# Optimization experiments

Measured on AMD Instinct MI355X. Metric: run time of the kernel, lower is better.

## Reference

```python
import jax, jax.numpy as jnp
import numpy as np
import math

B, S, H, DK = 16, 4096, 16, 64
DM = H * DK          # 1024, d_model
QD = 1024            # q_d_model
KVD = 1024           # kv_d_model
MASK_P = 0.85        # randbool probability


def setup_inputs() -> dict:
    key = jax.random.key(0)
    ks = jax.random.split(key, 12)
    s = 0.02
    return {
        "q": jax.random.normal(ks[0], (B, 1, QD), jnp.float32),
        "k": jax.random.normal(ks[1], (B, S, KVD), jnp.float32),
        "v": jax.random.normal(ks[2], (B, S, KVD), jnp.float32),
        "Wq": jax.random.normal(ks[3], (QD, DM), jnp.float32) * s,
        "bq": jnp.zeros((DM,), jnp.float32),
        "Wk": jax.random.normal(ks[4], (KVD, DM), jnp.float32) * s,
        "bk": jnp.zeros((DM,), jnp.float32),
        "Wv": jax.random.normal(ks[5], (KVD, DM), jnp.float32) * s,
        "bv": jnp.zeros((DM,), jnp.float32),
        "Wo": jax.random.normal(ks[6], (DM, QD), jnp.float32) * s,
        "bo": jnp.zeros((QD,), jnp.float32),
        # randbool(shape, p=0.85): True where rand < p -> score zeroed
        "maskfill": jax.random.uniform(ks[7], (B, H, 1, S)) < MASK_P,
    }


def reference(q, k, v, Wq, bq, Wk, bk, Wv, bv, Wo, bo, maskfill):
    bs = q.shape[0]
    # projections -> [B, L, H, DK] -> [B, H, L, DK]
    qh = (q @ Wq + bq).reshape(bs, -1, H, DK).transpose(0, 2, 1, 3)  # [B,H,1,DK]
    kh = (k @ Wk + bk).reshape(bs, -1, H, DK).transpose(0, 2, 1, 3)  # [B,H,S,DK]
    vh = (v @ Wv + bv).reshape(bs, -1, H, DK).transpose(0, 2, 1, 3)  # [B,H,S,DK]

    scores1 = jnp.einsum("bhqd,bhkd->bhqk", qh, kh) / math.sqrt(DK)  # [B,H,1,S]

    # plain path (dropout = identity in eval)
    attn = jax.nn.softmax(scores1, axis=-1)
    out_h = jnp.einsum("bhqk,bhkd->bhqd", attn, vh)                  # [B,H,1,DK]

    # masked path: zero-fill (not -inf) masked raw scores, then softmax
    masked_scores = jnp.where(maskfill, 0.0, scores1)
    mattn = jax.nn.softmax(masked_scores, axis=-1)
    mout_h = jnp.einsum("bhqk,bhkd->bhqd", mattn, vh)

    concat = out_h.transpose(0, 2, 1, 3).reshape(bs, DM)
    mconcat = mout_h.transpose(0, 2, 1, 3).reshape(bs, DM)
    output = concat @ Wo + bo
    masked_output = mconcat @ Wo + bo
    return (output, masked_output)
```

## Files before the change

kernel.cpp:

```cpp
#include <hip/hip_runtime.h>
#include <stdint.h>

#define NB 16
#define NS 4096
#define NH 16
#define NC 1024

#define OFF_QHP   0u
#define OFF_QK    262144u
#define OFF_QB    524288u
#define OFF_SP    524608u
#define OFF_CTXP  532800u
#define OFF_CON   8921408u

__global__ __launch_bounds__(128) void k_qh(
    const float* __restrict__ q, const float* __restrict__ Wq, float* __restrict__ qhp)
{
    __shared__ float qs[64*16];
    int dz = blockIdx.x, cs = blockIdx.y;
    int tid = threadIdx.x;
    int d = dz*128 + tid;
#pragma unroll
    for (int j = 0; j < 2; ++j) {
        int idx = j*128 + tid;
        int b = idx >> 4, c4 = (idx & 15) << 2;
        float4 t = *(const float4*)(q + (size_t)b*NC + cs*64 + c4);
        qs[(c4+0)*16 + b] = t.x; qs[(c4+1)*16 + b] = t.y;
        qs[(c4+2)*16 + b] = t.z; qs[(c4+3)*16 + b] = t.w;
    }
    __syncthreads();
    float acc[16];
#pragma unroll
    for (int b = 0; b < 16; ++b) acc[b] = 0.f;
#pragma unroll 4
    for (int c = 0; c < 64; ++c) {
        float w = Wq[(size_t)(cs*64 + c)*NC + d];
        const float4* qr = (const float4*)(qs + c*16);
        float4 q0 = qr[0], q1 = qr[1], q2 = qr[2], q3 = qr[3];
        acc[0]  = fmaf(w, q0.x, acc[0]);  acc[1]  = fmaf(w, q0.y, acc[1]);
        acc[2]  = fmaf(w, q0.z, acc[2]);  acc[3]  = fmaf(w, q0.w, acc[3]);
        acc[4]  = fmaf(w, q1.x, acc[4]);  acc[5]  = fmaf(w, q1.y, acc[5]);
        acc[6]  = fmaf(w, q1.z, acc[6]);  acc[7]  = fmaf(w, q1.w, acc[7]);
        acc[8]  = fmaf(w, q2.x, acc[8]);  acc[9]  = fmaf(w, q2.y, acc[9]);
        acc[10] = fmaf(w, q2.z, acc[10]); acc[11] = fmaf(w, q2.w, acc[11]);
        acc[12] = fmaf(w, q3.x, acc[12]); acc[13] = fmaf(w, q3.y, acc[13]);
        acc[14] = fmaf(w, q3.z, acc[14]); acc[15] = fmaf(w, q3.w, acc[15]);
    }
#pragma unroll
    for (int b = 0; b < 16; ++b) qhp[((size_t)cs*16 + b)*NC + d] = acc[b];
}

__global__ __launch_bounds__(128) void k_qk(
    const float* __restrict__ qhp, const float* __restrict__ bq,
    const float* __restrict__ Wk, const float* __restrict__ bk,
    float* __restrict__ qko, float* __restrict__ qbv)
{
    int h = blockIdx.x;
    int c = blockIdx.y*128 + threadIdx.x;
    __shared__ float qs[16*64];
    for (int j = 0; j < 8; ++j) {
        int idx = j*128 + threadIdx.x;
        int b = idx >> 6, dd = idx & 63;
        float a = bq[h*64 + dd];
#pragma unroll
        for (int cs = 0; cs < 16; ++cs) a += qhp[((size_t)cs*16 + b)*NC + h*64 + dd];
        qs[idx] = a;
    }
    __syncthreads();
    const float* wr = Wk + (size_t)c*NC + h*64;
    float acc[16];
#pragma unroll
    for (int b = 0; b < 16; ++b) acc[b] = 0.f;
#pragma unroll 4
    for (int d = 0; d < 64; ++d) {
        float w = wr[d];
#pragma unroll
        for (int b = 0; b < 16; ++b) acc[b] = fmaf(qs[b*64 + d], w, acc[b]);
    }
#pragma unroll
    for (int b = 0; b < 16; ++b) qko[((size_t)b*NH + h)*NC + c] = acc[b];
    if (blockIdx.y == 0 && threadIdx.x < 16) {
        int b = threadIdx.x; float a = 0.f;
        for (int d = 0; d < 64; ++d) a = fmaf(qs[b*64 + d], bk[h*64 + d], a);
        qbv[b*NH + h] = a;
    }
}

#define QTS 20
#define SCOMP(BUF, W)                                                          \
    _Pragma("unroll")                                                          \
    for (int j = 0; j < 4; ++j) {                                              \
        const float* qp = qt + ((W)*16 + ph*4 + j)*QTS + hg*4;                 \
        float4 qv = *(const float4*)qp;                                        \
        _Pragma("unroll")                                                      \
        for (int i = 0; i < 8; ++i) {                                          \
            float kc = (j == 0) ? BUF[i].x : (j == 1) ? BUF[i].y               \
                     : (j == 2) ? BUF[i].z : BUF[i].w;                         \
            acc[i][0] = fmaf(kc, qv.x, acc[i][0]);                             \
            acc[i][1] = fmaf(kc, qv.y, acc[i][1]);                             \
            acc[i][2] = fmaf(kc, qv.z, acc[i][2]);                             \
            acc[i][3] = fmaf(kc, qv.w, acc[i][3]);                             \
        }                                                                      \
    }
__global__ __launch_bounds__(512, 2) void k_att(
    const float* __restrict__ kk, const float* __restrict__ vv,
    const float* __restrict__ qkm, const float* __restrict__ qbv,
    const void* __restrict__ mask, float* __restrict__ ctxp, float* __restrict__ Sp)
{
    __shared__ float qt[512*QTS];
    __shared__ float attl[256*32];
    __shared__ float red[8][2][16];
    int sb = blockIdx.x, b = blockIdx.y;
    int tid = threadIdx.x;
    int ph = tid & 3, hg = (tid >> 2) & 3, rg = tid >> 4;
    int srow = sb*256 + rg*8;

    int fl;
    {
        const uint4* mw = (const uint4*)mask;
        unsigned f = 0u, g = 0u;
#pragma unroll
        for (int j = 0; j < 8; ++j) {
            uint4 m4 = mw[j];
            f |= (m4.x == 0x3F800000u) | (m4.y == 0x3F800000u)
               | (m4.z == 0x3F800000u) | (m4.w == 0x3F800000u);
            g |= ((m4.x > 1u) & (m4.x != 0x3F800000u))
               | ((m4.y > 1u) & (m4.y != 0x3F800000u))
               | ((m4.z > 1u) & (m4.z != 0x3F800000u))
               | ((m4.w > 1u) & (m4.w != 0x3F800000u));
        }
        fl = f ? 2 : (g ? 1 : 0);
    }

    const float* kr = kk + ((size_t)b*NS + srow)*NC + ph*4;
    float acc[8][4];
#pragma unroll
    for (int i = 0; i < 8; ++i)
#pragma unroll
        for (int j = 0; j < 4; ++j) acc[i][j] = 0.f;

    for (int cz = 0; cz < 2; ++cz) {
        __syncthreads();
#pragma unroll
        for (int j = 0; j < 16; ++j) {
            int idx = j*512 + tid;
            int h = idx >> 9, c = idx & 511;
            qt[c*QTS + h] = qkm[((size_t)b*NH + h)*NC + cz*512 + c];
        }
        __syncthreads();
        const float* kc0 = kr + cz*512;
        float4 A[8], B[8], T[8];
#pragma unroll
        for (int i = 0; i < 8; ++i) A[i] = *(const float4*)(kc0 + i*NC);
#pragma unroll
        for (int i = 0; i < 8; ++i) B[i] = *(const float4*)(kc0 + i*NC + 16);
        for (int w = 0; w < 32; w += 2) {
            if (w + 2 < 32) {
#pragma unroll
                for (int i = 0; i < 8; ++i)
                    T[i] = *(const float4*)(kc0 + i*NC + (w+2)*16);
            }
            SCOMP(A, w);
            if (w + 3 < 32) {
#pragma unroll
                for (int i = 0; i < 8; ++i)
                    A[i] = *(const float4*)(kc0 + i*NC + (w+3)*16);
            }
            SCOMP(B, (w+1));
#pragma unroll
            for (int i = 0; i < 8; ++i) { B[i] = A[i]; A[i] = T[i]; }
        }
    }
#pragma unroll
    for (int i = 0; i < 8; ++i)
#pragma unroll
        for (int j = 0; j < 4; ++j) {
            acc[i][j] += __shfl_xor(acc[i][j], 1, 64);
            acc[i][j] += __shfl_xor(acc[i][j], 2, 64);
        }
    float d0[4], d1[4];
    if (ph == 0) {
#pragma unroll
        for (int j = 0; j < 4; ++j) { d0[j] = acc[0][j]; d1[j] = acc[1][j]; }
    } else if (ph == 1) {
#pragma unroll
        for (int j = 0; j < 4; ++j) { d0[j] = acc[2][j]; d1[j] = acc[3][j]; }
    } else if (ph == 2) {
#pragma unroll
        for (int j = 0; j < 4; ++j) { d0[j] = acc[4][j]; d1[j] = acc[5][j]; }
    } else {
#pragma unroll
        for (int j = 0; j < 4; ++j) { d0[j] = acc[6][j]; d1[j] = acc[7][j]; }
    }
    int lA = rg*8 + 2*ph, lB = lA + 1;
    int sA = sb*256 + lA, sB = sA + 1;
    unsigned mA = 0, mB = 0;
    if (fl == 1) {
        const uint8_t* mp = (const uint8_t*)mask + (size_t)(b*NH + hg*4)*NS;
#pragma unroll
        for (int j = 0; j < 4; ++j) {
            if (mp[(size_t)j*NS + sA]) mA |= (1u << j);
            if (mp[(size_t)j*NS + sB]) mB |= (1u << j);
        }
    } else if (fl == 2) {
        const float* mp = (const float*)mask + (size_t)(b*NH + hg*4)*NS;
#pragma unroll
        for (int j = 0; j < 4; ++j) {
            if (mp[(size_t)j*NS + sA] != 0.f) mA |= (1u << j);
            if (mp[(size_t)j*NS + sB] != 0.f) mB |= (1u << j);
        }
    } else {
        const int* mp = (const int*)mask + (size_t)(b*NH + hg*4)*NS;
#pragma unroll
        for (int j = 0; j < 4; ++j) {
            if (mp[(size_t)j*NS + sA]) mA |= (1u << j);
            if (mp[(size_t)j*NS + sB]) mB |= (1u << j);
        }
    }
    float p0a[4], p1a[4], p0b[4], p1b[4], r0[4], r1[4];
#pragma unroll
    for (int j = 0; j < 4; ++j) {
        float qb = qbv[b*NH + hg*4 + j];
        float va = (d0[j] + qb) * 0.125f;
        float vb2 = (d1[j] + qb) * 0.125f;
        p0a[j] = __expf(va);  p1a[j] = (mA >> j & 1u) ? 1.0f : p0a[j];
        p0b[j] = __expf(vb2); p1b[j] = (mB >> j & 1u) ? 1.0f : p0b[j];
        r0[j] = p0a[j] + p0b[j];
        r1[j] = p1a[j] + p1b[j];
    }
    {
        int swA = (lA & 7) << 2, swB = (lB & 7) << 2;
        *(float4*)(attl + lA*32 + ((hg*4) ^ swA))        = make_float4(p0a[0], p0a[1], p0a[2], p0a[3]);
        *(float4*)(attl + lA*32 + ((16 + hg*4) ^ swA))   = make_float4(p1a[0], p1a[1], p1a[2], p1a[3]);
        *(float4*)(attl + lB*32 + ((hg*4) ^ swB))        = make_float4(p0b[0], p0b[1], p0b[2], p0b[3]);
        *(float4*)(attl + lB*32 + ((16 + hg*4) ^ swB))   = make_float4(p1b[0], p1b[1], p1b[2], p1b[3]);
    }
#pragma unroll
    for (int j = 0; j < 4; ++j) {
        r0[j] += __shfl_xor(r0[j], 1, 64);  r1[j] += __shfl_xor(r1[j], 1, 64);
        r0[j] += __shfl_xor(r0[j], 2, 64);  r1[j] += __shfl_xor(r1[j], 2, 64);
        r0[j] += __shfl_xor(r0[j], 16, 64); r1[j] += __shfl_xor(r1[j], 16, 64);
        r0[j] += __shfl_xor(r0[j], 32, 64); r1[j] += __shfl_xor(r1[j], 32, 64);
    }
    int wv = tid >> 6;
    if ((tid & 51) == 0) {
#pragma unroll
        for (int j = 0; j < 4; ++j) {
            red[wv][0][hg*4 + j] = r0[j];
            red[wv][1][hg*4 + j] = r1[j];
        }
    }
    __syncthreads();
    if (tid < 32) {
        int pa = tid >> 4, h = tid & 15;
        float a = 0.f;
#pragma unroll
        for (int w8 = 0; w8 < 8; ++w8) a += red[w8][pa][h];
        Sp[((size_t)b*16 + sb)*32 + tid] = a;
    }

    int cq = tid & 255, half = tid >> 8;
    float cacc[16][4];
#pragma unroll
    for (int u = 0; u < 16; ++u)
#pragma unroll
        for (int j = 0; j < 4; ++j) cacc[u][j] = 0.f;
    const float* vb = vv + ((size_t)b*NS + sb*256)*NC + cq*4;
    float4 vr[8], vn[8];
#pragma unroll
    for (int i = 0; i < 8; ++i) vr[i] = *(const float4*)(vb + (size_t)i*NC);
    for (int r0q = 0; r0q < 256; r0q += 8) {
        if (r0q + 8 < 256) {
#pragma unroll
            for (int i = 0; i < 8; ++i)
                vn[i] = *(const float4*)(vb + (size_t)(r0q + 8 + i)*NC);
        }
#pragma unroll
        for (int i = 0; i < 8; ++i) {
            int r = r0q + i;
            const float* ar = attl + r*32;
            int lw = r & 7;
            float4 vcur = vr[i];
#pragma unroll
            for (int g = 0; g < 4; ++g) {
                int G = half*4 + g;
                float4 aw = *(const float4*)(ar + ((G ^ lw) << 2));
                cacc[g*4+0][0] = fmaf(aw.x, vcur.x, cacc[g*4+0][0]);
                cacc[g*4+0][1] = fmaf(aw.x, vcur.y, cacc[g*4+0][1]);
                cacc[g*4+0][2] = fmaf(aw.x, vcur.z, cacc[g*4+0][2]);
                cacc[g*4+0][3] = fmaf(aw.x, vcur.w, cacc[g*4+0][3]);
                cacc[g*4+1][0] = fmaf(aw.y, vcur.x, cacc[g*4+1][0]);
                cacc[g*4+1][1] = fmaf(aw.y, vcur.y, cacc[g*4+1][1]);
                cacc[g*4+1][2] = fmaf(aw.y, vcur.z, cacc[g*4+1][2]);
                cacc[g*4+1][3] = fmaf(aw.y, vcur.w, cacc[g*4+1][3]);
                cacc[g*4+2][0] = fmaf(aw.z, vcur.x, cacc[g*4+2][0]);
                cacc[g*4+2][1] = fmaf(aw.z, vcur.y, cacc[g*4+2][1]);
                cacc[g*4+2][2] = fmaf(aw.z, vcur.z, cacc[g*4+2][2]);
                cacc[g*4+2][3] = fmaf(aw.z, vcur.w, cacc[g*4+2][3]);
                cacc[g*4+3][0] = fmaf(aw.w, vcur.x, cacc[g*4+3][0]);
                cacc[g*4+3][1] = fmaf(aw.w, vcur.y, cacc[g*4+3][1]);
                cacc[g*4+3][2] = fmaf(aw.w, vcur.z, cacc[g*4+3][2]);
                cacc[g*4+3][3] = fmaf(aw.w, vcur.w, cacc[g*4+3][3]);
            }
        }
#pragma unroll
        for (int i = 0; i < 8; ++i) vr[i] = vn[i];
    }
#pragma unroll
    for (int gh = 0; gh < 16; ++gh) {
        *(float4*)(ctxp + ((((size_t)sb*2 + half)*NB + b)*NH + gh)*NC + cq*4)
            = make_float4(cacc[gh][0], cacc[gh][1], cacc[gh][2], cacc[gh][3]);
    }
}

__global__ __launch_bounds__(256) void k_outhN(
    const float* __restrict__ ctxp, const float* __restrict__ Sp,
    const float* __restrict__ Wv, const float* __restrict__ bv,
    float* __restrict__ con)
{
    int b = blockIdx.y, p = blockIdx.z;
    int dx = blockIdx.x;
    int d = dx*256 + threadIdx.x;
    int h0 = dx*4;
    __shared__ float cl[4*NC];
    float Sinv[4];
#pragma unroll
    for (int j = 0; j < 4; ++j) {
        float a = 0.f;
        for (int sb = 0; sb < 16; ++sb)
            a += Sp[((size_t)b*16 + sb)*32 + p*16 + h0 + j];
        Sinv[j] = 1.f / a;
    }
#pragma unroll
    for (int hh = 0; hh < 4; ++hh) {
        for (int cc = threadIdx.x; cc < NC; cc += 256) {
            float a = 0.f;
#pragma unroll
            for (int ss = 0; ss < 16; ++ss)
                a += ctxp[((((size_t)ss*2 + p)*NB + b)*NH + h0 + hh)*NC + cc];
            cl[hh*NC + cc] = a * Sinv[hh];
        }
    }
    __syncthreads();
    const float* c2 = cl + ((threadIdx.x >> 6) << 10);
    float a0=0.f,a1=0.f,a2=0.f,a3=0.f;
    for (int c = 0; c < NC; c += 4) {
        a0 = fmaf(c2[c+0], Wv[(size_t)(c+0)*NC + d], a0);
        a1 = fmaf(c2[c+1], Wv[(size_t)(c+1)*NC + d], a1);
        a2 = fmaf(c2[c+2], Wv[(size_t)(c+2)*NC + d], a2);
        a3 = fmaf(c2[c+3], Wv[(size_t)(c+3)*NC + d], a3);
    }
    con[((size_t)p*NB + b)*NC + d] = (a0+a1)+(a2+a3) + bv[d];
}

__global__ __launch_bounds__(256) void k_out(
    const float* __restrict__ con, const float* __restrict__ Wo,
    const float* __restrict__ bo, float* __restrict__ out)
{
    int b = blockIdx.y, p = blockIdx.z;
    int o = blockIdx.x*256 + threadIdx.x;
    __shared__ float cl[NC];
    for (int i = threadIdx.x; i < NC; i += 256)
        cl[i] = con[((size_t)p*NB + b)*NC + i];
    __syncthreads();
    float a0=0.f,a1=0.f,a2=0.f,a3=0.f;
    for (int m = 0; m < NC; m += 4) {
        a0 = fmaf(cl[m+0], Wo[(size_t)(m+0)*NC + o], a0);
        a1 = fmaf(cl[m+1], Wo[(size_t)(m+1)*NC + o], a1);
        a2 = fmaf(cl[m+2], Wo[(size_t)(m+2)*NC + o], a2);
        a3 = fmaf(cl[m+3], Wo[(size_t)(m+3)*NC + o], a3);
    }
    out[(size_t)p*NB*NC + (size_t)b*NC + o] = (a0+a1)+(a2+a3) + bo[o];
}

extern "C" void kernel_launch(void* const* d_in, const int* in_sizes, int n_in,
                              void* d_out, int out_size, void* d_ws, size_t ws_size,
                              hipStream_t stream)
{
    (void)in_sizes; (void)n_in; (void)out_size; (void)ws_size;
    const float* q  = (const float*)d_in[0];
    const float* k  = (const float*)d_in[1];
    const float* v  = (const float*)d_in[2];
    const float* Wq = (const float*)d_in[3];
    const float* bq = (const float*)d_in[4];
    const float* Wk = (const float*)d_in[5];
    const float* bk = (const float*)d_in[6];
    const float* Wv = (const float*)d_in[7];
    const float* bv = (const float*)d_in[8];
    const float* Wo = (const float*)d_in[9];
    const float* bo = (const float*)d_in[10];
    const void*  mk = d_in[11];

    float* ws   = (float*)d_ws;
    float* qhp  = ws + OFF_QHP;
    float* qkv  = ws + OFF_QK;
    float* qbv  = ws + OFF_QB;
    float* Sp   = ws + OFF_SP;
    float* ctxp = ws + OFF_CTXP;
    float* con  = ws + OFF_CON;
    float* out  = (float*)d_out;

    k_qh<<<dim3(8, 16), 128, 0, stream>>>(q, Wq, qhp);
    k_qk<<<dim3(16, 8), 128, 0, stream>>>(qhp, bq, Wk, bk, qkv, qbv);
    k_att<<<dim3(16, 16), 512, 0, stream>>>(k, v, qkv, qbv, mk, ctxp, Sp);
    k_outhN<<<dim3(4, NB, 2), 256, 0, stream>>>(ctxp, Sp, Wv, bv, con);
    k_out<<<dim3(4, NB, 2), 256, 0, stream>>>(con, Wo, bo, out);
}
```

Baseline: 251.3 us.

## Halve attention rows per block to double grid size and raise occupancy

```diff
diff --git a/kernel.cpp b/kernel.cpp
--- a/kernel.cpp
+++ b/kernel.cpp
@@ -9,9 +9,9 @@
 #define OFF_QHP   0u
 #define OFF_QK    262144u
 #define OFF_QB    524288u
-#define OFF_SP    524608u
-#define OFF_CTXP  532800u
-#define OFF_CON   8921408u
+#define OFF_SP    524544u
+#define OFF_CTXP  540928u
+#define OFF_CON   17318144u
 
 __global__ __launch_bounds__(128) void k_qh(
     const float* __restrict__ q, const float* __restrict__ Wq, float* __restrict__ qhp)
@@ -93,7 +93,7 @@
         const float* qp = qt + ((W)*16 + ph*4 + j)*QTS + hg*4;                 \
         float4 qv = *(const float4*)qp;                                        \
         _Pragma("unroll")                                                      \
-        for (int i = 0; i < 8; ++i) {                                          \
+        for (int i = 0; i < 4; ++i) {                                          \
             float kc = (j == 0) ? BUF[i].x : (j == 1) ? BUF[i].y               \
                      : (j == 2) ? BUF[i].z : BUF[i].w;                         \
             acc[i][0] = fmaf(kc, qv.x, acc[i][0]);                             \
@@ -102,18 +102,18 @@
             acc[i][3] = fmaf(kc, qv.w, acc[i][3]);                             \
         }                                                                      \
     }
-__global__ __launch_bounds__(512, 2) void k_att(
+__global__ __launch_bounds__(512, 4) void k_att(
     const float* __restrict__ kk, const float* __restrict__ vv,
     const float* __restrict__ qkm, const float* __restrict__ qbv,
     const void* __restrict__ mask, float* __restrict__ ctxp, float* __restrict__ Sp)
 {
     __shared__ float qt[512*QTS];
-    __shared__ float attl[256*32];
+    __shared__ float attl[128*32];
     __shared__ float red[8][2][16];
     int sb = blockIdx.x, b = blockIdx.y;
     int tid = threadIdx.x;
     int ph = tid & 3, hg = (tid >> 2) & 3, rg = tid >> 4;
-    int srow = sb*256 + rg*8;
+    int srow = sb*128 + rg*4;
 
     int fl;
     {
@@ -133,9 +133,9 @@
     }
 
     const float* kr = kk + ((size_t)b*NS + srow)*NC + ph*4;
-    float acc[8][4];
-#pragma unroll
-    for (int i = 0; i < 8; ++i)
+    float acc[4][4];
+#pragma unroll
+    for (int i = 0; i < 4; ++i)
 #pragma unroll
         for (int j = 0; j < 4; ++j) acc[i][j] = 0.f;
 
@@ -149,91 +149,82 @@
         }
         __syncthreads();
         const float* kc0 = kr + cz*512;
-        float4 A[8], B[8], T[8];
-#pragma unroll
-        for (int i = 0; i < 8; ++i) A[i] = *(const float4*)(kc0 + i*NC);
-#pragma unroll
-        for (int i = 0; i < 8; ++i) B[i] = *(const float4*)(kc0 + i*NC + 16);
+        float4 A[4], B[4], T[4];
+#pragma unroll
+        for (int i = 0; i < 4; ++i) A[i] = *(const float4*)(kc0 + i*NC);
+#pragma unroll
+        for (int i = 0; i < 4; ++i) B[i] = *(const float4*)(kc0 + i*NC + 16);
         for (int w = 0; w < 32; w += 2) {
             if (w + 2 < 32) {
 #pragma unroll
-                for (int i = 0; i < 8; ++i)
+                for (int i = 0; i < 4; ++i)
                     T[i] = *(const float4*)(kc0 + i*NC + (w+2)*16);
             }
             SCOMP(A, w);
             if (w + 3 < 32) {
 #pragma unroll
-                for (int i = 0; i < 8; ++i)
+                for (int i = 0; i < 4; ++i)
                     A[i] = *(const float4*)(kc0 + i*NC + (w+3)*16);
             }
             SCOMP(B, (w+1));
 #pragma unroll
-            for (int i = 0; i < 8; ++i) { B[i] = A[i]; A[i] = T[i]; }
-        }
-    }
-#pragma unroll
-    for (int i = 0; i < 8; ++i)
+            for (int i = 0; i < 4; ++i) { B[i] = A[i]; A[i] = T[i]; }
+        }
+    }
+#pragma unroll
+    for (int i = 0; i < 4; ++i)
 #pragma unroll
         for (int j = 0; j < 4; ++j) {
             acc[i][j] += __shfl_xor(acc[i][j], 1, 64);
             acc[i][j] += __shfl_xor(acc[i][j], 2, 64);
         }
-    float d0[4], d1[4];
+    float d0[4];
     if (ph == 0) {
 #pragma unroll
-        for (int j = 0; j < 4; ++j) { d0[j] = acc[0][j]; d1[j] = acc[1][j]; }
+        for (int j = 0; j < 4; ++j) d0[j] = acc[0][j];
     } else if (ph == 1) {
 #pragma unroll
-        for (int j = 0; j < 4; ++j) { d0[j] = acc[2][j]; d1[j] = acc[3][j]; }
+        for (int j = 0; j < 4; ++j) d0[j] = acc[1][j];
     } else if (ph == 2) {
 #pragma unroll
-        for (int j = 0; j < 4; ++j) { d0[j] = acc[4][j]; d1[j] = acc[5][j]; }
+        for (int j = 0; j < 4; ++j) d0[j] = acc[2][j];
     } else {
 #pragma unroll
-        for (int j = 0; j < 4; ++j) { d0[j] = acc[6][j]; d1[j] = acc[7][j]; }
-    }
-    int lA = rg*8 + 2*ph, lB = lA + 1;
-    int sA = sb*256 + lA, sB = sA + 1;
-    unsigned mA = 0, mB = 0;
+        for (int j = 0; j < 4; ++j) d0[j] = acc[3][j];
+    }
+    int lA = rg*4 + ph;
+    int sA = sb*128 + lA;
+    unsigned mA = 0;
     if (fl == 1) {
         const uint8_t* mp = (const uint8_t*)mask + (size_t)(b*NH + hg*4)*NS;
 #pragma unroll
-        for (int j = 0; j < 4; ++j) {
+        for (int j = 0; j < 4; ++j)
             if (mp[(size_t)j*NS + sA]) mA |= (1u << j);
-            if (mp[(size_t)j*NS + sB]) mB |= (1u << j);
-        }
     } else if (fl == 2) {
         const float* mp = (const float*)mask + (size_t)(b*NH + hg*4)*NS;
 #pragma unroll
-        for (int j = 0; j < 4; ++j) {
+        for (int j = 0; j < 4; ++j)
             if (mp[(size_t)j*NS + sA] != 0.f) mA |= (1u << j);
-            if (mp[(size_t)j*NS + sB] != 0.f) mB |= (1u << j);
-        }
     } else {
         const int* mp = (const int*)mask + (size_t)(b*NH + hg*4)*NS;
 #pragma unroll
-        for (int j = 0; j < 4; ++j) {
+        for (int j = 0; j < 4; ++j)
             if (mp[(size_t)j*NS + sA]) mA |= (1u << j);
-            if (mp[(size_t)j*NS + sB]) mB |= (1u << j);
-        }
-    }
-    float p0a[4], p1a[4], p0b[4], p1b[4], r0[4], r1[4];
+    }
+    float p0a[4], p1a[4], r0[4], r1[4];
 #pragma unroll
     for (int j = 0; j < 4; ++j) {
         float qb = qbv[b*NH + hg*4 + j];
         float va = (d0[j] + qb) * 0.125f;
-        float vb2 = (d1[j] + qb) * 0.125f;
-        p0a[j] = __expf(va);  p1a[j] = (mA >> j & 1u) ? 1.0f : p0a[j];
-        p0b[j] = __expf(vb2); p1b[j] = (mB >> j & 1u) ? 1.0f : p0b[j];
-        r0[j] = p0a[j] + p0b[j];
-        r1[j] = p1a[j] + p1b[j];
+        p0a[j] = __expf(va);
+        p1a[j] = (mA >> j & 1u) ? 1.0f : p0a[j];
+        r0[j] = p0a[j];
+        r1[j] = p1a[j];
     }
     {
-        int swA = (lA & 7) << 2, swB = (lB & 7) << 2;
-        *(float4*)(attl + lA*32 + ((hg*4) ^ swA))        = make_float4(p0a[0], p0a[1], p0a[2], p0a[3]);
-        *(float4*)(attl + lA*32 + ((16 + hg*4) ^ swA))   = make_float4(p1a[0], p1a[1], p1a[2], p1a[3]);
-        *(float4*)(attl + lB*32 + ((hg*4) ^ swB))        = make_float4(p0b[0], p0b[1], p0b[2], p0b[3]);
-        *(float4*)(attl + lB*32 + ((16 + hg*4) ^ swB))   = make_float4(p1b[0], p1b[1], p1b[2], p1b[3]);
+        int swA = (lA & 7) << 2;
+        *(float4*)(attl + lA*32 + ((hg*4) ^ swA))      = make_float4(p0a[0], p0a[1], p0a[2], p0a[3]);
+        *(float4*)(attl + lA*32 + ((16 + hg*4) ^ swA)) = make_float4(p1a[0], p1a[1], p1a[2], p1a[3]);
     }
 #pragma unroll
     for (int j = 0; j < 4; ++j) {
@@ -256,7 +247,7 @@
         float a = 0.f;
 #pragma unroll
         for (int w8 = 0; w8 < 8; ++w8) a += red[w8][pa][h];
-        Sp[((size_t)b*16 + sb)*32 + tid] = a;
+        Sp[((size_t)b*32 + sb)*32 + tid] = a;
     }
 
     int cq = tid & 255, half = tid >> 8;
@@ -265,12 +256,12 @@
     for (int u = 0; u < 16; ++u)
 #pragma unroll
         for (int j = 0; j < 4; ++j) cacc[u][j] = 0.f;
-    const float* vb = vv + ((size_t)b*NS + sb*256)*NC + cq*4;
+    const float* vb = vv + ((size_t)b*NS + sb*128)*NC + cq*4;
     float4 vr[8], vn[8];
 #pragma unroll
     for (int i = 0; i < 8; ++i) vr[i] = *(const float4*)(vb + (size_t)i*NC);
-    for (int r0q = 0; r0q < 256; r0q += 8) {
-        if (r0q + 8 < 256) {
+    for (int r0q = 0; r0q < 128; r0q += 8) {
+        if (r0q + 8 < 128) {
 #pragma unroll
             for (int i = 0; i < 8; ++i)
                 vn[i] = *(const float4*)(vb + (size_t)(r0q + 8 + i)*NC);
@@ -327,8 +318,8 @@
 #pragma unroll
     for (int j = 0; j < 4; ++j) {
         float a = 0.f;
-        for (int sb = 0; sb < 16; ++sb)
-            a += Sp[((size_t)b*16 + sb)*32 + p*16 + h0 + j];
+        for (int sb = 0; sb < 32; ++sb)
+            a += Sp[((size_t)b*32 + sb)*32 + p*16 + h0 + j];
         Sinv[j] = 1.f / a;
     }
 #pragma unroll
@@ -336,7 +327,7 @@
         for (int cc = threadIdx.x; cc < NC; cc += 256) {
             float a = 0.f;
 #pragma unroll
-            for (int ss = 0; ss < 16; ++ss)
+            for (int ss = 0; ss < 32; ++ss)
                 a += ctxp[((((size_t)ss*2 + p)*NB + b)*NH + h0 + hh)*NC + cc];
             cl[hh*NC + cc] = a * Sinv[hh];
         }
@@ -402,7 +393,7 @@
 
     k_qh<<<dim3(8, 16), 128, 0, stream>>>(q, Wq, qhp);
     k_qk<<<dim3(16, 8), 128, 0, stream>>>(qhp, bq, Wk, bk, qkv, qbv);
-    k_att<<<dim3(16, 16), 512, 0, stream>>>(k, v, qkv, qbv, mk, ctxp, Sp);
+    k_att<<<dim3(32, 16), 512, 0, stream>>>(k, v, qkv, qbv, mk, ctxp, Sp);
     k_outhN<<<dim3(4, NB, 2), 256, 0, stream>>>(ctxp, Sp, Wv, bv, con);
     k_out<<<dim3(4, NB, 2), 256, 0, stream>>>(con, Wo, bo, out);
 }
```

Measured after the change: 467.2 us. 1.86x slower.
